# Performance work log

Hardware: AMD Instinct MI355X
Metric: run time of the kernel (lower is better)

The kernel has to match this reference:

```python
import jax, jax.numpy as jnp
import numpy as np

NUM_BUCKETS = 32
MAX_DISTANCE = 128
N_HEADS = 16
D_KV = 64


def relative_position_bucket(rel, num_buckets=NUM_BUCKETS, max_distance=MAX_DISTANCE):
    # bidirectional (encoder) bucketing, matches the torch reference
    nb = num_buckets // 2
    ret = (rel > 0).astype(jnp.int32) * nb
    rp = jnp.abs(rel)
    max_exact = nb // 2
    is_small = rp < max_exact
    # guard log(0); masked out by is_small anyway
    large = max_exact + (
        jnp.log(jnp.maximum(rp, 1).astype(jnp.float32) / max_exact)
        / np.log(max_distance / max_exact)
        * (nb - max_exact)
    ).astype(jnp.int32)
    large = jnp.minimum(large, nb - 1)
    return ret + jnp.where(is_small, rp, large)


def compute_bias(rel_bias_table, q_len, k_len):
    q_pos = jnp.arange(q_len)[:, None]
    k_pos = jnp.arange(k_len)[None, :]
    buckets = relative_position_bucket(k_pos - q_pos)  # [S, K]
    bias = rel_bias_table[buckets]                      # [S, K, H]
    return jnp.transpose(bias, (2, 0, 1))[None]         # [1, H, S, K]


def setup_inputs() -> dict:
    key = jax.random.key(0)
    ks = jax.random.split(key, 6)
    d_model, inner = 1024, N_HEADS * D_KV
    scale = 1.0 / np.sqrt(d_model)
    return {
        "hidden_states": jax.random.normal(ks[0], (4, 2048, d_model), jnp.float32),
        "Wq": jax.random.normal(ks[1], (d_model, inner), jnp.float32) * scale,
        "Wk": jax.random.normal(ks[2], (d_model, inner), jnp.float32) * scale,
        "Wv": jax.random.normal(ks[3], (d_model, inner), jnp.float32) * scale,
        "Wo": jax.random.normal(ks[4], (inner, d_model), jnp.float32) * scale,
        "rel_bias_table": jax.random.normal(ks[5], (NUM_BUCKETS, N_HEADS), jnp.float32),
    }


def reference(hidden_states, Wq, Wk, Wv, Wo, rel_bias_table):
    B, S, _ = hidden_states.shape
    K_len = S  # self-attention (key_value_states is None)
    q = (hidden_states @ Wq).reshape(B, S, N_HEADS, D_KV)
    k = (hidden_states @ Wk).reshape(B, K_len, N_HEADS, D_KV)
    v = (hidden_states @ Wv).reshape(B, K_len, N_HEADS, D_KV)
    # NOTE: T5 attention has no 1/sqrt(d_kv) scaling
    scores = jnp.einsum("bshd,bkhd->bhsk", q, k)
    pos_bias = compute_bias(rel_bias_table, S, K_len)
    attn = jax.nn.softmax(scores + pos_bias, axis=-1)
    out = jnp.einsum("bhsk,bkhd->bshd", attn, v).reshape(B, S, N_HEADS * D_KV)
    out = out @ Wo
    return (out, pos_bias)
```

## Files before the change

kernel.cpp:

```cpp
#include <hip/hip_runtime.h>
#include <cstdint>
#include <cstddef>

typedef unsigned short u16;
typedef unsigned int u32;
typedef __attribute__((ext_vector_type(8))) short bf16x8;
typedef __attribute__((ext_vector_type(4))) float f32x4;
typedef __attribute__((ext_vector_type(16))) float f32x16;

#define MFMA(a, b, c)   __builtin_amdgcn_mfma_f32_16x16x32_bf16((a), (b), (c), 0, 0, 0)
#define MFMA32(a, b, c) __builtin_amdgcn_mfma_f32_32x32x16_bf16((a), (b), (c), 0, 0, 0)

typedef const __attribute__((address_space(1))) void gv1_t;
typedef __attribute__((address_space(3))) void lv3_t;
#define GLOAD_LDS16(g, l) __builtin_amdgcn_global_load_lds((gv1_t*)(g), (lv3_t*)(l), 16, 0, 0)

#define BATCH 4
#define SEQ 2048
#define DMODEL 1024
#define NHEAD 16
#define MROWS (BATCH * SEQ)
#define QKVN (3 * DMODEL)

#define LOG2E 1.44269504088896340736f

__device__ __forceinline__ u16 f2bf(float f) {
  u32 x = __builtin_bit_cast(u32, f);
  x += 0x7fffu + ((x >> 16) & 1u);
  return (u16)(x >> 16);
}

__device__ __forceinline__ u32 pkbf(float a, float b) {
  return (u32)f2bf(a) | ((u32)f2bf(b) << 16);
}

extern "C" __device__ float __ocml_exp2_f32(float);
__device__ __forceinline__ float exp2fast(float x) {
#if __has_builtin(__builtin_amdgcn_exp2f)
  return __builtin_amdgcn_exp2f(x);
#else
  return __ocml_exp2_f32(x);
#endif
}

__global__ __launch_bounds__(256) void convert_h(const float* __restrict__ H,
                                                 u16* __restrict__ Hb) {
  size_t i = (size_t)blockIdx.x * 1024 + threadIdx.x * 4;
  float4 v = *(const float4*)&H[i];
  uint2 o;
  o.x = pkbf(v.x, v.y);
  o.y = pkbf(v.z, v.w);
  *(uint2*)&Hb[i] = o;
}

__global__ void transpose_w(const float* __restrict__ Wq, const float* __restrict__ Wk,
                            const float* __restrict__ Wv, const float* __restrict__ Wo,
                            u16* __restrict__ Wt) {
  __shared__ u16 Ts[32][33];
  const float* W = (blockIdx.z == 0) ? Wq : (blockIdx.z == 1) ? Wk
                   : (blockIdx.z == 2) ? Wv : Wo;
  const float s = (blockIdx.z == 0) ? LOG2E : 1.0f;
  int x = threadIdx.x, y0 = threadIdx.y;
  int r0 = blockIdx.y * 32, c0 = blockIdx.x * 32;
  for (int yy = y0; yy < 32; yy += 8)
    Ts[yy][x] = f2bf(W[(size_t)(r0 + yy) * 1024 + c0 + x] * s);
  __syncthreads();
  for (int yy = y0; yy < 32; yy += 8)
    Wt[(size_t)(blockIdx.z * 1024 + c0 + yy) * 1024 + r0 + x] = Ts[x][yy];
}

__device__ __forceinline__ int rel_bucket(int rel) {
  int ret = (rel > 0) ? 16 : 0;
  int rp = (rel < 0) ? -rel : rel;
  if (rp < 8) return ret + rp;
  int i = 0;
  i += (rp >= 12); i += (rp >= 16); i += (rp >= 23); i += (rp >= 32);
  i += (rp >= 46); i += (rp >= 64); i += (rp >= 91);
  return ret + 8 + i;
}

__global__ __launch_bounds__(256) void build_bias_rel(const float* __restrict__ tbl,
                                                      float* __restrict__ brel,
                                                      float* __restrict__ brel2) {
  int h = blockIdx.x;
  for (int rix = threadIdx.x; rix < 4095; rix += 256) {
    float v = tbl[rel_bucket(rix - 2047) * NHEAD + h];
    brel[h * 4096 + rix] = v;
    brel2[h * 4096 + rix] = v * LOG2E;
  }
}

__global__ __launch_bounds__(256) void gemm_bf16k(const u16* __restrict__ A,
                                                  const u16* __restrict__ Bt,
                                                  u16* __restrict__ Cb, float* __restrict__ Cf,
                                                  int M, int N, int K) {
  __shared__ u16 As[128 * 32];
  __shared__ u16 Bs[128 * 32];
  const int t = threadIdx.x;
  const int w = t >> 6, lane = t & 63, quad = lane >> 4, l15 = lane & 15;
  const int wr = w >> 1, wc = w & 1;
  const int row0 = blockIdx.y * 128, col0 = blockIdx.x * 128;

  f32x4 acc[4][4];
  #pragma unroll
  for (int i = 0; i < 4; ++i)
    #pragma unroll
    for (int j = 0; j < 4; ++j) acc[i][j] = (f32x4){0.f, 0.f, 0.f, 0.f};

  const int srow = lane >> 2, scol = (lane & 3) * 8;

  for (int k0 = 0; k0 < K; k0 += 32) {
    #pragma unroll
    for (int p = 0; p < 2; ++p) {
      const int rb = w * 32 + p * 16;
      GLOAD_LDS16(&A[(size_t)(row0 + rb + srow) * K + k0 + scol], &As[rb * 32]);
      GLOAD_LDS16(&Bt[(size_t)(col0 + rb + srow) * K + k0 + scol], &Bs[rb * 32]);
    }
    __syncthreads();
    bf16x8 af[4], bfr[4];
    #pragma unroll
    for (int i = 0; i < 4; ++i)
      af[i] = *(const bf16x8*)&As[(wr * 64 + i * 16 + l15) * 32 + quad * 8];
    #pragma unroll
    for (int j = 0; j < 4; ++j)
      bfr[j] = *(const bf16x8*)&Bs[(wc * 64 + j * 16 + l15) * 32 + quad * 8];
    #pragma unroll
    for (int i = 0; i < 4; ++i)
      #pragma unroll
      for (int j = 0; j < 4; ++j)
        acc[i][j] = MFMA(af[i], bfr[j], acc[i][j]);
    __syncthreads();
  }
  #pragma unroll
  for (int i = 0; i < 4; ++i) {
    #pragma unroll
    for (int j = 0; j < 4; ++j) {
      int col = col0 + wc * 64 + j * 16 + l15;
      #pragma unroll
      for (int r = 0; r < 4; ++r) {
        int row = row0 + wr * 64 + i * 16 + quad * 4 + r;
        if (Cb) Cb[(size_t)row * N + col] = f2bf(acc[i][j][r]);
        else    Cf[(size_t)row * N + col] = acc[i][j][r];
      }
    }
  }
}

__global__ __launch_bounds__(256) void transpose_v(const u16* __restrict__ QKV,
                                                   u16* __restrict__ Vt) {
  __shared__ u16 Ts[64 * 72];
  int st = blockIdx.x, bh = blockIdx.y;
  int b = bh >> 4, h = bh & 15;
  int t = threadIdx.x;
  #pragma unroll
  for (int p = 0; p < 2; ++p) {
    int c = t * 2 + p, r = c >> 3, cc = (c & 7) * 8;
    *(uint4*)&Ts[r * 72 + cc] =
        *(const uint4*)&QKV[(size_t)(b * SEQ + st * 64 + r) * QKVN + 2 * DMODEL + h * 64 + cc];
  }
  __syncthreads();
  #pragma unroll
  for (int p = 0; p < 2; ++p) {
    int c = t * 2 + p, d = c >> 3, s8 = (c & 7) * 8;
    union { u16 u[8]; uint4 v; } tmp;
    #pragma unroll
    for (int jj = 0; jj < 8; ++jj) tmp.u[jj] = Ts[(s8 + jj) * 72 + d];
    *(uint4*)&Vt[((size_t)(bh * 64 + d)) * SEQ + st * 64 + s8] = tmp.v;
  }
}

__global__ __launch_bounds__(256) void attn_fused(const u16* __restrict__ QKV,
                                                  const u16* __restrict__ Vt,
                                                  const float* __restrict__ brel,
                                                  const float* __restrict__ brel2,
                                                  u16* __restrict__ Aout,
                                                  float* __restrict__ pb) {
  __shared__ u16 Ks[64 * 72];
  __shared__ u16 Vs[64 * 72];
  __shared__ u16 Ps[4][32 * 72];
  const int qt = blockIdx.x, bh = blockIdx.y;
  const int b = bh >> 4, h = bh & 15;
  const int t = threadIdx.x;
  const int w = t >> 6, lane = t & 63, l31 = lane & 31, h5 = lane >> 5;
  const int qb = qt * 128;
  const int qw0 = qb + w * 32;
  const int qr = qw0 + l31;
  const bool wrbias = (bh < 16);

  const float cpos = brel2[h * 4096 + 4040];
  const float cneg = brel2[h * 4096 + 54];
  const float cpu  = brel[h * 4096 + 4040];
  const float cnu  = brel[h * 4096 + 54];

  const u16* qptr = QKV + (size_t)(b * SEQ + qr) * QKVN + h * 64 + h5 * 8;
  bf16x8 qf[4];
  #pragma unroll
  for (int ks = 0; ks < 4; ++ks) qf[ks] = *(const bf16x8*)(qptr + ks * 16);

  float lsum = 0.f;
  f32x16 oacc[2];
  #pragma unroll
  for (int m = 0; m < 2; ++m)
    #pragma unroll
    for (int i = 0; i < 16; ++i) oacc[m][i] = 0.f;

  const int c0 = t * 2, c1 = c0 + 1;
  const int r0s = c0 >> 3, cc0 = (c0 & 7) * 8;
  const int r1s = c1 >> 3, cc1 = (c1 & 7) * 8;
  const size_t krow = (size_t)(b * SEQ) * QKVN + DMODEL + h * 64;
  const size_t vtrow = (size_t)bh * 64;
  const float* brow = brel2 + h * 4096 + 2047;
  u16* Pw = Ps[w];

  uint4 ka0 = *(const uint4*)&QKV[krow + (size_t)r0s * QKVN + cc0];
  uint4 ka1 = *(const uint4*)&QKV[krow + (size_t)r1s * QKVN + cc1];
  uint4 va0 = *(const uint4*)&Vt[(vtrow + r0s) * SEQ + cc0];
  uint4 va1 = *(const uint4*)&Vt[(vtrow + r1s) * SEQ + cc1];

  for (int kb = 0; kb < SEQ; kb += 64) {
    *(uint4*)&Ks[r0s * 72 + cc0] = ka0;
    *(uint4*)&Ks[r1s * 72 + cc1] = ka1;
    *(uint4*)&Vs[r0s * 72 + cc0] = va0;
    *(uint4*)&Vs[r1s * 72 + cc1] = va1;
    __syncthreads();

    if (kb + 64 < SEQ) {
      ka0 = *(const uint4*)&QKV[krow + (size_t)(kb + 64 + r0s) * QKVN + cc0];
      ka1 = *(const uint4*)&QKV[krow + (size_t)(kb + 64 + r1s) * QKVN + cc1];
      va0 = *(const uint4*)&Vt[(vtrow + r0s) * SEQ + kb + 64 + cc0];
      va1 = *(const uint4*)&Vt[(vtrow + r1s) * SEQ + kb + 64 + cc1];
    }

    f32x16 sc[2];
    #pragma unroll
    for (int m = 0; m < 2; ++m) {
      #pragma unroll
      for (int i = 0; i < 16; ++i) sc[m][i] = 0.f;
      #pragma unroll
      for (int ks = 0; ks < 4; ++ks) {
        bf16x8 kf = *(const bf16x8*)&Ks[(m * 32 + l31) * 72 + ks * 16 + h5 * 8];
        sc[m] = MFMA32(kf, qf[ks], sc[m]);
      }
    }

    if (wrbias) {
      const int pr = qb + (t >> 1);
      const int pc = kb + (t & 1) * 32;
      float* po = pb + ((size_t)(h * SEQ + pr)) * SEQ + pc;
      const int lo = pc - pr;
      if (lo >= 91 || lo + 31 <= -91) {
        const float c = (lo >= 91) ? cpu : cnu;
        const float4 vv = {c, c, c, c};
        #pragma unroll
        for (int i = 0; i < 8; ++i) *(float4*)&po[i * 4] = vv;
      } else {
        const float* bb = brel + h * 4096 + 2047 - pr + pc;
        #pragma unroll
        for (int i = 0; i < 8; ++i) {
          float4 vv;
          vv.x = bb[i * 4]; vv.y = bb[i * 4 + 1];
          vv.z = bb[i * 4 + 2]; vv.w = bb[i * 4 + 3];
          *(float4*)&po[i * 4] = vv;
        }
      }
    }

    #pragma unroll
    for (int m = 0; m < 2; ++m) {
      const int kb32 = kb + 32 * m;
      if (kb32 >= qw0 + 122) {
        #pragma unroll
        for (int i = 0; i < 16; ++i) sc[m][i] += cpos;
      } else if (kb32 <= qw0 - 122) {
        #pragma unroll
        for (int i = 0; i < 16; ++i) sc[m][i] += cneg;
      } else {
        const float* bb = brow + kb32 + 4 * h5 - qr;
        #pragma unroll
        for (int i = 0; i < 16; ++i) sc[m][i] += bb[(i & 3) + 8 * (i >> 2)];
      }
      #pragma unroll
      for (int tt = 0; tt < 4; ++tt) {
        float p0 = exp2fast(sc[m][4 * tt + 0]);
        float p1 = exp2fast(sc[m][4 * tt + 1]);
        float p2 = exp2fast(sc[m][4 * tt + 2]);
        float p3 = exp2fast(sc[m][4 * tt + 3]);
        lsum += (p0 + p1) + (p2 + p3);
        uint2 pk;
        pk.x = pkbf(p0, p1);
        pk.y = pkbf(p2, p3);
        *(uint2*)&Pw[l31 * 72 + 32 * m + 8 * tt + 4 * h5] = pk;
      }
    }

    asm volatile("s_waitcnt lgkmcnt(0)" ::: "memory");
    bf16x8 bp[4];
    #pragma unroll
    for (int ks = 0; ks < 4; ++ks)
      bp[ks] = *(const bf16x8*)&Pw[l31 * 72 + ks * 16 + h5 * 8];
    #pragma unroll
    for (int m2 = 0; m2 < 2; ++m2)
      #pragma unroll
      for (int ks = 0; ks < 4; ++ks) {
        bf16x8 vf = *(const bf16x8*)&Vs[(m2 * 32 + l31) * 72 + ks * 16 + h5 * 8];
        oacc[m2] = MFMA32(vf, bp[ks], oacc[m2]);
      }
    __syncthreads();
  }

  lsum += __shfl_xor(lsum, 32);
  const float inv = 1.0f / lsum;
  const size_t rowb = (size_t)(b * SEQ + qr) * DMODEL + h * 64;
  #pragma unroll
  for (int m2 = 0; m2 < 2; ++m2)
    #pragma unroll
    for (int tt = 0; tt < 4; ++tt) {
      uint2 o;
      o.x = pkbf(oacc[m2][4 * tt + 0] * inv, oacc[m2][4 * tt + 1] * inv);
      o.y = pkbf(oacc[m2][4 * tt + 2] * inv, oacc[m2][4 * tt + 3] * inv);
      *(uint2*)&Aout[rowb + 32 * m2 + 8 * tt + 4 * h5] = o;
    }
}

extern "C" void kernel_launch(void* const* d_in, const int* in_sizes, int n_in,
                              void* d_out, int out_size, void* d_ws, size_t ws_size,
                              hipStream_t stream) {
  (void)in_sizes; (void)n_in; (void)out_size; (void)ws_size;
  const float* H   = (const float*)d_in[0];
  const float* Wq  = (const float*)d_in[1];
  const float* Wk  = (const float*)d_in[2];
  const float* Wv  = (const float*)d_in[3];
  const float* Wo  = (const float*)d_in[4];
  const float* tbl = (const float*)d_in[5];

  float* out = (float*)d_out;
  float* pos_bias = out + (size_t)MROWS * DMODEL;

  char* ws = (char*)d_ws;
  u16* Hb     = (u16*)(ws);
  u16* Wt     = (u16*)(ws + 16777216);
  u16* QKV    = (u16*)(ws + 25165824);
  u16* Vt     = (u16*)(ws + 75497472);
  float* brel  = (float*)(ws + 92274688);
  float* brel2 = (float*)(ws + 92536832);

  convert_h<<<8192, 256, 0, stream>>>(H, Hb);
  transpose_w<<<dim3(32, 32, 4), dim3(32, 8), 0, stream>>>(Wq, Wk, Wv, Wo, Wt);
  build_bias_rel<<<16, 256, 0, stream>>>(tbl, brel, brel2);

  gemm_bf16k<<<dim3(QKVN / 128, MROWS / 128), 256, 0, stream>>>(
      Hb, Wt, QKV, nullptr, MROWS, QKVN, DMODEL);
  transpose_v<<<dim3(32, 64), 256, 0, stream>>>(QKV, Vt);
  attn_fused<<<dim3(16, 64), 256, 0, stream>>>(QKV, Vt, brel, brel2,
                                               Hb , pos_bias);
  gemm_bf16k<<<dim3(DMODEL / 128, MROWS / 128), 256, 0, stream>>>(
      Hb, Wt + (size_t)QKVN * DMODEL, nullptr, out, MROWS, DMODEL, DMODEL);
}
```

Baseline: 682.2 us.

## Use permlane32 swap for P fragments, GEMM swizzle, nontemporal stores, setprio

The attention kernel no longer stages softmax probabilities through per-wave LDS. It rebuilds the B-operand fragments in registers with permlane32_swap, which removes the LDS writes, the wait and the reads. The GEMM also remaps workgroup IDs across 8 groups, likely to improve L2 locality across chiplets. The fp32 output and the large position-bias writes now use nontemporal stores, and s_setprio is raised around the MFMA blocks. The register-level fragment permutation must exactly match the old LDS layout to stay correct.

```diff
diff --git a/kernel.cpp b/kernel.cpp
--- a/kernel.cpp
+++ b/kernel.cpp
@@ -7,6 +7,7 @@
 typedef __attribute__((ext_vector_type(8))) short bf16x8;
 typedef __attribute__((ext_vector_type(4))) float f32x4;
 typedef __attribute__((ext_vector_type(16))) float f32x16;
+typedef __attribute__((ext_vector_type(2))) unsigned int u32x2;
 
 #define MFMA(a, b, c)   __builtin_amdgcn_mfma_f32_16x16x32_bf16((a), (b), (c), 0, 0, 0)
 #define MFMA32(a, b, c) __builtin_amdgcn_mfma_f32_32x32x16_bf16((a), (b), (c), 0, 0, 0)
@@ -32,6 +33,10 @@
 
 __device__ __forceinline__ u32 pkbf(float a, float b) {
   return (u32)f2bf(a) | ((u32)f2bf(b) << 16);
+}
+
+__device__ __forceinline__ u32x2 plswap(u32 a, u32 b) {
+  return __builtin_amdgcn_permlane32_swap(a, b, false, false);
 }
 
 extern "C" __device__ float __ocml_exp2_f32(float);
@@ -99,7 +104,12 @@
   const int t = threadIdx.x;
   const int w = t >> 6, lane = t & 63, quad = lane >> 4, l15 = lane & 15;
   const int wr = w >> 1, wc = w & 1;
-  const int row0 = blockIdx.y * 128, col0 = blockIdx.x * 128;
+
+  const int nwg = gridDim.x * gridDim.y;
+  const int orig = blockIdx.y * gridDim.x + blockIdx.x;
+  const int wg = (orig & 7) * (nwg >> 3) + (orig >> 3);
+  const int bx = wg % gridDim.x, by = wg / gridDim.x;
+  const int row0 = by * 128, col0 = bx * 128;
 
   f32x4 acc[4][4];
   #pragma unroll
@@ -140,7 +150,7 @@
       for (int r = 0; r < 4; ++r) {
         int row = row0 + wr * 64 + i * 16 + quad * 4 + r;
         if (Cb) Cb[(size_t)row * N + col] = f2bf(acc[i][j][r]);
-        else    Cf[(size_t)row * N + col] = acc[i][j][r];
+        else    __builtin_nontemporal_store(acc[i][j][r], &Cf[(size_t)row * N + col]);
       }
     }
   }
@@ -177,7 +187,6 @@
                                                   float* __restrict__ pb) {
   __shared__ u16 Ks[64 * 72];
   __shared__ u16 Vs[64 * 72];
-  __shared__ u16 Ps[4][32 * 72];
   const int qt = blockIdx.x, bh = blockIdx.y;
   const int b = bh >> 4, h = bh & 15;
   const int t = threadIdx.x;
@@ -210,7 +219,6 @@
   const size_t krow = (size_t)(b * SEQ) * QKVN + DMODEL + h * 64;
   const size_t vtrow = (size_t)bh * 64;
   const float* brow = brel2 + h * 4096 + 2047;
-  u16* Pw = Ps[w];
 
   uint4 ka0 = *(const uint4*)&QKV[krow + (size_t)r0s * QKVN + cc0];
   uint4 ka1 = *(const uint4*)&QKV[krow + (size_t)r1s * QKVN + cc1];
@@ -232,6 +240,7 @@
     }
 
     f32x16 sc[2];
+    __builtin_amdgcn_s_setprio(1);
     #pragma unroll
     for (int m = 0; m < 2; ++m) {
       #pragma unroll
@@ -242,6 +251,7 @@
         sc[m] = MFMA32(kf, qf[ks], sc[m]);
       }
     }
+    __builtin_amdgcn_s_setprio(0);
 
     if (wrbias) {
       const int pr = qb + (t >> 1);
@@ -250,21 +260,23 @@
       const int lo = pc - pr;
       if (lo >= 91 || lo + 31 <= -91) {
         const float c = (lo >= 91) ? cpu : cnu;
-        const float4 vv = {c, c, c, c};
-        #pragma unroll
-        for (int i = 0; i < 8; ++i) *(float4*)&po[i * 4] = vv;
+        const f32x4 vv = {c, c, c, c};
+        #pragma unroll
+        for (int i = 0; i < 8; ++i)
+          __builtin_nontemporal_store(vv, (f32x4*)&po[i * 4]);
       } else {
         const float* bb = brel + h * 4096 + 2047 - pr + pc;
         #pragma unroll
         for (int i = 0; i < 8; ++i) {
-          float4 vv;
+          f32x4 vv;
           vv.x = bb[i * 4]; vv.y = bb[i * 4 + 1];
           vv.z = bb[i * 4 + 2]; vv.w = bb[i * 4 + 3];
-          *(float4*)&po[i * 4] = vv;
+          __builtin_nontemporal_store(vv, (f32x4*)&po[i * 4]);
         }
       }
     }
 
+    bf16x8 bp[4];
     #pragma unroll
     for (int m = 0; m < 2; ++m) {
       const int kb32 = kb + 32 * m;
@@ -279,6 +291,7 @@
         #pragma unroll
         for (int i = 0; i < 16; ++i) sc[m][i] += bb[(i & 3) + 8 * (i >> 2)];
       }
+      u32 w0[4], w1[4];
       #pragma unroll
       for (int tt = 0; tt < 4; ++tt) {
         float p0 = exp2fast(sc[m][4 * tt + 0]);
@@ -286,18 +299,21 @@
         float p2 = exp2fast(sc[m][4 * tt + 2]);
         float p3 = exp2fast(sc[m][4 * tt + 3]);
         lsum += (p0 + p1) + (p2 + p3);
-        uint2 pk;
-        pk.x = pkbf(p0, p1);
-        pk.y = pkbf(p2, p3);
-        *(uint2*)&Pw[l31 * 72 + 32 * m + 8 * tt + 4 * h5] = pk;
-      }
-    }
-
-    asm volatile("s_waitcnt lgkmcnt(0)" ::: "memory");
-    bf16x8 bp[4];
-    #pragma unroll
-    for (int ks = 0; ks < 4; ++ks)
-      bp[ks] = *(const bf16x8*)&Pw[l31 * 72 + ks * 16 + h5 * 8];
+        w0[tt] = pkbf(p0, p1);
+        w1[tt] = pkbf(p2, p3);
+      }
+      u32x2 r0 = plswap(w0[0], w0[1]);
+      u32x2 r1 = plswap(w1[0], w1[1]);
+      u32x2 r2 = plswap(w0[2], w0[3]);
+      u32x2 r3 = plswap(w1[2], w1[3]);
+      union { u32 u[4]; bf16x8 v; } q0, q1;
+      q0.u[0] = r0.x; q0.u[1] = r1.x; q0.u[2] = r0.y; q0.u[3] = r1.y;
+      q1.u[0] = r2.x; q1.u[1] = r3.x; q1.u[2] = r2.y; q1.u[3] = r3.y;
+      bp[2 * m]     = q0.v;
+      bp[2 * m + 1] = q1.v;
+    }
+
+    __builtin_amdgcn_s_setprio(1);
     #pragma unroll
     for (int m2 = 0; m2 < 2; ++m2)
       #pragma unroll
@@ -305,6 +321,7 @@
         bf16x8 vf = *(const bf16x8*)&Vs[(m2 * 32 + l31) * 72 + ks * 16 + h5 * 8];
         oacc[m2] = MFMA32(vf, bp[ks], oacc[m2]);
       }
+    __builtin_amdgcn_s_setprio(0);
     __syncthreads();
   }
 
```

Measured after the change: 1.329 ms. +94.9%, slower.
